# Kernel tuning notes

Hardware: AMD Instinct MI355X
Metric: run time of the kernel (lower is better)

Reference implementation:

```python
import jax, jax.numpy as jnp
import numpy as np

D_MODEL = 1024
N_HEADS = 16
HEAD = D_MODEL // N_HEADS  # 64


def setup_inputs() -> dict:
    key = jax.random.key(0)
    ks = jax.random.split(key, 9)
    s = 1.0 / np.sqrt(D_MODEL)
    x = jax.random.normal(ks[0], (2, 2048, D_MODEL), dtype=jnp.float32)
    Wq = jax.random.uniform(ks[1], (N_HEADS, D_MODEL, HEAD), jnp.float32, -s, s)
    bq = jax.random.uniform(ks[2], (N_HEADS, HEAD), jnp.float32, -s, s)
    Wk = jax.random.uniform(ks[3], (N_HEADS, D_MODEL, HEAD), jnp.float32, -s, s)
    bk = jax.random.uniform(ks[4], (N_HEADS, HEAD), jnp.float32, -s, s)
    Wv = jax.random.uniform(ks[5], (N_HEADS, D_MODEL, HEAD), jnp.float32, -s, s)
    bv = jax.random.uniform(ks[6], (N_HEADS, HEAD), jnp.float32, -s, s)
    Wo = jax.random.uniform(ks[7], (D_MODEL, D_MODEL), jnp.float32, -s, s)
    bo = jax.random.uniform(ks[8], (D_MODEL,), jnp.float32, -s, s)
    return {"x": x, "Wq": Wq, "bq": bq, "Wk": Wk, "bk": bk,
            "Wv": Wv, "bv": bv, "Wo": Wo, "bo": bo}


def reference(x, Wq, bq, Wk, bk, Wv, bv, Wo, bo):
    # Per-head projections, vectorized over heads: [B,S,D] x [H,D,h] -> [B,H,S,h]
    Q = jnp.einsum('bsd,hdk->bhsk', x, Wq) + bq[None, :, None, :]
    K = jnp.einsum('bsd,hdk->bhsk', x, Wk) + bk[None, :, None, :]
    V = jnp.einsum('bsd,hdk->bhsk', x, Wv) + bv[None, :, None, :]
    scores = jnp.einsum('bhqk,bhsk->bhqs', Q, K) / jnp.sqrt(jnp.float32(HEAD))
    attn = jax.nn.softmax(scores, axis=-1)  # dropout is identity in eval mode
    out = jnp.einsum('bhqs,bhsk->bhqk', attn, V)  # [B,H,S,h]
    B, H, S, h = out.shape
    out = out.transpose(0, 2, 1, 3).reshape(B, S, H * h)  # concat heads -> [B,S,D]
    return out @ Wo.T + bo if False else jnp.einsum('bsd,ed->bse', out, Wo.T.T) + bo
```

## Files before the change

kernel.cpp:

```cpp
#include <hip/hip_runtime.h>
#include <hip/hip_bf16.h>

typedef unsigned short u16;
typedef short short8 __attribute__((ext_vector_type(8)));
typedef float floatx4 __attribute__((ext_vector_type(4)));

#define MFMA16(a, b, c) __builtin_amdgcn_mfma_f32_16x16x32_bf16((a), (b), (c), 0, 0, 0)

union U128u { uint4 q; u16 s[8]; };

__device__ __forceinline__ u16 f2bf(float f) {
  union { float f; unsigned u; } v; v.f = f;
  unsigned r = v.u + 0x7fffu + ((v.u >> 16) & 1u);
  return (u16)(r >> 16);
}

__device__ __forceinline__ float bf2f(u16 s) {
  union { unsigned u; float f; } v; v.u = ((unsigned)s) << 16;
  return v.f;
}

__device__ __forceinline__ unsigned pk2(float hi, float lo) {
  union { float f; unsigned u; } a, b;
  a.f = hi; b.f = lo;
  return __builtin_amdgcn_perm(a.u + 0x8000u, b.u + 0x8000u, 0x07060302u);
}

__device__ __forceinline__ float fexp2(float x) {
#if __has_builtin(__builtin_amdgcn_exp2f)
  return __builtin_amdgcn_exp2f(x);
#else
  return exp2f(x);
#endif
}

__device__ __forceinline__ void async16(const u16* g, u16* l) {
  __builtin_amdgcn_global_load_lds(
      (const __attribute__((address_space(1))) unsigned int*)g,
      (__attribute__((address_space(3))) unsigned int*)l, 16, 0, 0);
}


__global__ __launch_bounds__(256) void prep_all(
    const float* __restrict__ x, const float* __restrict__ Wo,
    const float* __restrict__ Wq, const float* __restrict__ bq,
    const float* __restrict__ Wk, const float* __restrict__ bk,
    const float* __restrict__ Wv, const float* __restrict__ bv,
    u16* __restrict__ Xb, u16* __restrict__ Wob,
    u16* __restrict__ Wt, float* __restrict__ ball) {
  int bid = blockIdx.x;
  int tid = threadIdx.x;
  if (bid < 5120) {
    const float* src = bid < 4096 ? x : Wo;
    u16* dst = bid < 4096 ? Xb : Wob;
    int i = (bid < 4096 ? bid : bid - 4096) * 256 + tid;
    float4 v = ((const float4*)src)[i];
    union { unsigned long long ll; u16 s[4]; } o;
    o.s[0] = f2bf(v.x); o.s[1] = f2bf(v.y); o.s[2] = f2bf(v.z); o.s[3] = f2bf(v.w);
    ((unsigned long long*)dst)[i] = o.ll;
    return;
  }
  int id = (bid - 5120) * 256 + tid;
  int kk4 = id & 15;
  int d = (id >> 4) & 1023;
  int h = (id >> 14) & 15;
  int wsel = id >> 18;
  const float* W = wsel == 0 ? Wq : (wsel == 1 ? Wk : Wv);
  float4 v = *(const float4*)(W + ((size_t)(h * 1024 + d)) * 64 + kk4 * 4);
  int nb = wsel * 1024 + h * 64 + kk4 * 4;
  Wt[(size_t)(nb + 0) * 1024 + d] = f2bf(v.x);
  Wt[(size_t)(nb + 1) * 1024 + d] = f2bf(v.y);
  Wt[(size_t)(nb + 2) * 1024 + d] = f2bf(v.z);
  Wt[(size_t)(nb + 3) * 1024 + d] = f2bf(v.w);
  if (id < 3072) {
    int ws2 = id >> 10, hk = id & 1023;
    const float* bsrc = ws2 == 0 ? bq : (ws2 == 1 ? bk : bv);
    ball[id] = bsrc[hk];
  }
}

__global__ __launch_bounds__(256) void transpose_v(const u16* __restrict__ QKV,
                                                   u16* __restrict__ Vtc) {
  __shared__ u16 t[64][65];
  int tid = threadIdx.x;
  int bh = blockIdx.y, b = bh >> 4, h = bh & 15;
  int s0 = blockIdx.x * 64;
  int v0 = blockIdx.x * 4;
  {
    int r = tid >> 2, c0 = (tid & 3) * 16;
    const u16* src = QKV + (size_t)(b * 2048 + s0 + r) * 3072 + 2048 + h * 64 + c0;
    U128u a, c;
    a.q = *(const uint4*)src;
    c.q = *(const uint4*)(src + 8);
#pragma unroll
    for (int j = 0; j < 8; ++j) { t[r][c0 + j] = a.s[j]; t[r][c0 + 8 + j] = c.s[j]; }
  }
  __syncthreads();
  {
    int g = tid;
#pragma unroll
    for (int gg = 0; gg < 2; ++gg, g += 256) {
      int d = g & 63, o = (g >> 6) & 1, vloc = g >> 7;
      int sl = vloc * 16 + o * 8;
      U128u out;
#pragma unroll
      for (int k = 0; k < 8; ++k) out.s[k] = t[sl + k][d];
      u16* dst = Vtc + (((size_t)(bh * 128 + v0 + vloc) * 2 + o) * 64 + d) * 8;
      *(uint4*)dst = out.q;
    }
  }
}


__device__ __forceinline__ void store_out(u16* p, float v) { *p = f2bf(v); }
__device__ __forceinline__ void store_out(float* p, float v) { *p = v; }

template <int BN, typename OutT>
__global__ __launch_bounds__(256) void gemm_bt(
    const u16* __restrict__ A, const u16* __restrict__ B,
    const float* __restrict__ bias, OutT* __restrict__ C,
    int M, int N, int K, int scaleNend, float scaleVal) {
  constexpr int TN = BN / 32;
  __shared__ __attribute__((aligned(16))) u16 As[128 * 32];
  __shared__ __attribute__((aligned(16))) u16 Bs[BN * 32];
  const int tid = threadIdx.x;
  const int w = tid >> 6, lane = tid & 63;
  const int l15 = lane & 15, l4 = lane >> 4;
  const int lin = blockIdx.x;
  const int xcd = lin & 7, sblk = lin >> 3;
  const int bm = xcd * 4 + (sblk & 3);
  const int bn = sblk >> 2;
  const int wm = (w & 1) * 64, wn = (w >> 1) * (BN / 2);

  floatx4 acc[4][TN];
#pragma unroll
  for (int i = 0; i < 4; ++i)
#pragma unroll
    for (int j = 0; j < TN; ++j) acc[i][j] = (floatx4){0.f, 0.f, 0.f, 0.f};

  for (int k0 = 0; k0 < K; k0 += 32) {
    __syncthreads();
#pragma unroll
    for (int j = 0; j < 2; ++j) {
      int i = j * 256 + tid;
      int row = i >> 2, ko = (i & 3) * 8;
      async16(A + (size_t)(bm * 128 + row) * K + k0 + ko, As + (j * 256 + w * 64) * 8);
    }
#pragma unroll
    for (int j = 0; j < BN / 64; ++j) {
      int i = j * 256 + tid;
      int row = i >> 2, ko = (i & 3) * 8;
      async16(B + (size_t)(bn * BN + row) * K + k0 + ko, Bs + (j * 256 + w * 64) * 8);
    }
    __syncthreads();
    short8 af[4], bf[TN];
#pragma unroll
    for (int t = 0; t < 4; ++t)
      af[t] = *(const short8*)(As + (wm + t * 16 + l15) * 32 + l4 * 8);
#pragma unroll
    for (int t = 0; t < TN; ++t)
      bf[t] = *(const short8*)(Bs + (wn + t * 16 + l15) * 32 + l4 * 8);
#pragma unroll
    for (int tm = 0; tm < 4; ++tm)
#pragma unroll
      for (int tn = 0; tn < TN; ++tn) acc[tm][tn] = MFMA16(af[tm], bf[tn], acc[tm][tn]);
  }

#pragma unroll
  for (int tn = 0; tn < TN; ++tn) {
    int col = bn * BN + wn + tn * 16 + l15;
    float bv = bias[col];
    float sc = (col < scaleNend) ? scaleVal : 1.0f;
#pragma unroll
    for (int tm = 0; tm < 4; ++tm) {
      int row0 = bm * 128 + wm + tm * 16 + l4 * 4;
#pragma unroll
      for (int r = 0; r < 4; ++r) {
        float v = (acc[tm][tn][r] + bv) * sc;
        store_out(C + (size_t)(row0 + r) * N + col, v);
      }
    }
  }
}


__global__ __launch_bounds__(256, 3) void attn_kernel(const u16* __restrict__ QKV,
                                                      const u16* __restrict__ Vtc,
                                                      u16* __restrict__ Ob) {
  __shared__ __attribute__((aligned(16))) u16 lds[4 * 4736];
  const int tid = threadIdx.x;
  const int w = tid >> 6, lane = tid & 63;
  const int l15 = lane & 15, l4 = lane >> 4;
  const int lin = blockIdx.x;
  const int xcd = lin & 7, sblk = lin >> 3;
  const int bh = xcd * 4 + (sblk & 3);
  const int q0 = (sblk >> 2) * 64;
  const int b = bh >> 4, h = bh & 15;

  u16* const Pw = lds + w * 4736;

  short8 qf[4][2];
  {
    const u16* Qb = QKV + (size_t)(b * 2048 + q0) * 3072 + h * 64;
#pragma unroll
    for (int tq = 0; tq < 4; ++tq)
#pragma unroll
      for (int s = 0; s < 2; ++s)
        qf[tq][s] = *(const short8*)(Qb + (size_t)(tq * 16 + l15) * 3072 + s * 32 + l4 * 8);
  }

  floatx4 Oacc[4][4];
#pragma unroll
  for (int i = 0; i < 4; ++i)
#pragma unroll
    for (int j = 0; j < 4; ++j) Oacc[i][j] = (floatx4){0.f, 0.f, 0.f, 0.f};
  float lpart[4] = {0.f, 0.f, 0.f, 0.f};

  const u16* const Kb = QKV + (size_t)(b * 2048) * 3072 + 1024 + h * 64;
  const u16* const Vw = Vtc + (size_t)bh * 131072 + (size_t)w * 32768;
  const int kw0 = w * 512;

  for (int c = 0; c < 16; ++c) {
    const int key0 = kw0 + c * 32;
    short8 kf[2][2];
#pragma unroll
    for (int t = 0; t < 2; ++t)
#pragma unroll
      for (int s = 0; s < 2; ++s)
        kf[t][s] = *(const short8*)(Kb + (size_t)(key0 + t * 16 + l15) * 3072 + s * 32 + l4 * 8);
    short8 vf[4];
#pragma unroll
    for (int td = 0; td < 4; ++td)
      vf[td] = *(const short8*)(Vw + (size_t)c * 2048 + l4 * 512 + (td * 16 + l15) * 8);

#pragma unroll
    for (int t = 0; t < 2; ++t)
#pragma unroll
      for (int tq = 0; tq < 4; ++tq) {
        floatx4 s = (floatx4){0.f, 0.f, 0.f, 0.f};
        s = MFMA16(kf[t][0], qf[tq][0], s);
        s = MFMA16(kf[t][1], qf[tq][1], s);
        float p0 = fexp2(s[0]), p1 = fexp2(s[1]), p2 = fexp2(s[2]), p3 = fexp2(s[3]);
        lpart[tq] += (p0 + p1) + (p2 + p3);
        unsigned lo = pk2(p1, p0), hi = pk2(p3, p2);
        *(unsigned long long*)(Pw + (size_t)(tq * 16 + l15) * 40 + t * 16 + l4 * 4) =
            ((unsigned long long)hi << 32) | lo;
      }

    short8 pf[4];
#pragma unroll
    for (int tq = 0; tq < 4; ++tq)
      pf[tq] = *(const short8*)(Pw + (size_t)(tq * 16 + l15) * 40 + l4 * 8);
#pragma unroll
    for (int td = 0; td < 4; ++td)
#pragma unroll
      for (int tq = 0; tq < 4; ++tq) Oacc[tq][td] = MFMA16(pf[tq], vf[td], Oacc[tq][td]);
  }

  float lr[4];
#pragma unroll
  for (int tq = 0; tq < 4; ++tq) {
    float l = lpart[tq];
    l += __shfl_xor(l, 16);
    l += __shfl_xor(l, 32);
    lr[tq] = l;
  }

#pragma unroll
  for (int tq = 0; tq < 4; ++tq)
#pragma unroll
    for (int td = 0; td < 4; ++td)
#pragma unroll
      for (int r = 0; r < 4; ++r)
        Pw[(size_t)(tq * 16 + l4 * 4 + r) * 72 + td * 16 + l15] = f2bf(Oacc[tq][td][r]);
  if (l4 == 0) {
    float* Lw = (float*)(Pw + 4608);
#pragma unroll
    for (int tq = 0; tq < 4; ++tq) Lw[tq * 16 + l15] = lr[tq];
  }
  __syncthreads();

  {
    int row = tid >> 2, c0 = (tid & 3) * 16;
    float acc[16];
#pragma unroll
    for (int j = 0; j < 16; ++j) acc[j] = 0.f;
    float lsum = 0.f;
#pragma unroll
    for (int wv = 0; wv < 4; ++wv) {
      const u16* R = lds + wv * 4736;
      lsum += ((const float*)(R + 4608))[row];
      U128u x1, x2;
      x1.q = *(const uint4*)(R + (size_t)row * 72 + c0);
      x2.q = *(const uint4*)(R + (size_t)row * 72 + c0 + 8);
#pragma unroll
      for (int j = 0; j < 8; ++j) { acc[j] += bf2f(x1.s[j]); acc[8 + j] += bf2f(x2.s[j]); }
    }
    float inv = 1.0f / lsum;
    U128u o1, o2;
#pragma unroll
    for (int j = 0; j < 8; ++j) { o1.s[j] = f2bf(acc[j] * inv); o2.s[j] = f2bf(acc[8 + j] * inv); }
    u16* Op = Ob + (size_t)(b * 2048 + q0 + row) * 1024 + h * 64 + c0;
    *(uint4*)Op = o1.q;
    *(uint4*)(Op + 8) = o2.q;
  }
}


extern "C" void kernel_launch(void* const* d_in, const int* in_sizes, int n_in,
                              void* d_out, int out_size, void* d_ws, size_t ws_size,
                              hipStream_t stream) {
  const float* x  = (const float*)d_in[0];
  const float* Wq = (const float*)d_in[1];
  const float* bq = (const float*)d_in[2];
  const float* Wk = (const float*)d_in[3];
  const float* bk = (const float*)d_in[4];
  const float* Wv = (const float*)d_in[5];
  const float* bv = (const float*)d_in[6];
  const float* Wo = (const float*)d_in[7];
  const float* bo = (const float*)d_in[8];

  char* p = (char*)d_ws;
  u16* Xb   = (u16*)p; p += (size_t)4096 * 1024 * 2;
  u16* Wt   = (u16*)p; p += (size_t)3072 * 1024 * 2;
  u16* QKV  = (u16*)p; p += (size_t)4096 * 3072 * 2;
  u16* Vtc  = (u16*)p; p += (size_t)32 * 128 * 2 * 64 * 8 * 2;
  u16* Ob   = (u16*)p; p += (size_t)4096 * 1024 * 2;
  u16* Wob  = (u16*)p; p += (size_t)1024 * 1024 * 2;
  float* ball = (float*)p; p += 3072 * sizeof(float);

  const float qscale = 0.125f * 1.4426950408889634f;

  prep_all<<<8192, 256, 0, stream>>>(x, Wo, Wq, bq, Wk, bk, Wv, bv, Xb, Wob, Wt, ball);
  gemm_bt<128, u16><<<768, 256, 0, stream>>>(Xb, Wt, ball, QKV,
                                             4096, 3072, 1024, 1024, qscale);
  transpose_v<<<dim3(32, 32), 256, 0, stream>>>(QKV, Vtc);
  attn_kernel<<<1024, 256, 0, stream>>>(QKV, Vtc, Ob);
  gemm_bt<64, float><<<512, 256, 0, stream>>>(Ob, Wob, bo, (float*)d_out,
                                              4096, 1024, 1024, 0, 1.0f);
}
```

Before: 215.4 us.

## Feed softmax P directly into fp16 PV MFMA, removing LDS round-trip

```diff
diff --git a/kernel.cpp b/kernel.cpp
--- a/kernel.cpp
+++ b/kernel.cpp
@@ -4,10 +4,14 @@
 typedef unsigned short u16;
 typedef short short8 __attribute__((ext_vector_type(8)));
 typedef float floatx4 __attribute__((ext_vector_type(4)));
+typedef __fp16 half2v __attribute__((ext_vector_type(2)));
+typedef __fp16 half4v __attribute__((ext_vector_type(4)));
 
 #define MFMA16(a, b, c) __builtin_amdgcn_mfma_f32_16x16x32_bf16((a), (b), (c), 0, 0, 0)
+#define MFMA_PV(a, b, c) __builtin_amdgcn_mfma_f32_16x16x16f16((a), (b), (c), 0, 0, 0)
 
 union U128u { uint4 q; u16 s[8]; };
+union H4u { half4v h4; half2v h2[2]; unsigned u[2]; };
 
 __device__ __forceinline__ u16 f2bf(float f) {
   union { float f; unsigned u; } v; v.f = f;
@@ -18,12 +22,6 @@
 __device__ __forceinline__ float bf2f(u16 s) {
   union { unsigned u; float f; } v; v.u = ((unsigned)s) << 16;
   return v.f;
-}
-
-__device__ __forceinline__ unsigned pk2(float hi, float lo) {
-  union { float f; unsigned u; } a, b;
-  a.f = hi; b.f = lo;
-  return __builtin_amdgcn_perm(a.u + 0x8000u, b.u + 0x8000u, 0x07060302u);
 }
 
 __device__ __forceinline__ float fexp2(float x) {
@@ -80,7 +78,7 @@
 }
 
 __global__ __launch_bounds__(256) void transpose_v(const u16* __restrict__ QKV,
-                                                   u16* __restrict__ Vtc) {
+                                                   u16* __restrict__ VtF) {
   __shared__ u16 t[64][65];
   int tid = threadIdx.x;
   int bh = blockIdx.y, b = bh >> 4, h = bh & 15;
@@ -97,16 +95,19 @@
   }
   __syncthreads();
   {
-    int g = tid;
-#pragma unroll
-    for (int gg = 0; gg < 2; ++gg, g += 256) {
-      int d = g & 63, o = (g >> 6) & 1, vloc = g >> 7;
-      int sl = vloc * 16 + o * 8;
-      U128u out;
-#pragma unroll
-      for (int k = 0; k < 8; ++k) out.s[k] = t[sl + k][d];
-      u16* dst = Vtc + (((size_t)(bh * 128 + v0 + vloc) * 2 + o) * 64 + d) * 8;
-      *(uint4*)dst = out.q;
+    int d = tid & 63, vloc = tid >> 6;
+    int sl = vloc * 16;
+    u16* dst = VtF + ((size_t)(bh * 128 + v0 + vloc)) * 1024 + d * 4;
+#pragma unroll
+    for (int kq = 0; kq < 4; ++kq) {
+      float f0 = bf2f(t[sl + kq * 4 + 0][d]);
+      float f1 = bf2f(t[sl + kq * 4 + 1][d]);
+      float f2 = bf2f(t[sl + kq * 4 + 2][d]);
+      float f3 = bf2f(t[sl + kq * 4 + 3][d]);
+      union { half2v h2[2]; uint2 u2; } o;
+      o.h2[0] = __builtin_amdgcn_cvt_pkrtz(f0, f1);
+      o.h2[1] = __builtin_amdgcn_cvt_pkrtz(f2, f3);
+      *(uint2*)(dst + kq * 256) = o.u2;
     }
   }
 }
@@ -184,10 +185,10 @@
 }
 
 
-__global__ __launch_bounds__(256, 3) void attn_kernel(const u16* __restrict__ QKV,
-                                                      const u16* __restrict__ Vtc,
+__global__ __launch_bounds__(256, 4) void attn_kernel(const u16* __restrict__ QKV,
+                                                      const u16* __restrict__ VtF,
                                                       u16* __restrict__ Ob) {
-  __shared__ __attribute__((aligned(16))) u16 lds[4 * 4736];
+  __shared__ __attribute__((aligned(16))) u16 lds[4 * 2368];
   const int tid = threadIdx.x;
   const int w = tid >> 6, lane = tid & 63;
   const int l15 = lane & 15, l4 = lane >> 4;
@@ -196,103 +197,101 @@
   const int bh = xcd * 4 + (sblk & 3);
   const int q0 = (sblk >> 2) * 64;
   const int b = bh >> 4, h = bh & 15;
-
-  u16* const Pw = lds + w * 4736;
-
-  short8 qf[4][2];
+  const int qh = w >> 1, kh = w & 1;
+
+  short8 qf[2][2];
   {
-    const u16* Qb = QKV + (size_t)(b * 2048 + q0) * 3072 + h * 64;
-#pragma unroll
-    for (int tq = 0; tq < 4; ++tq)
+    const u16* Qb = QKV + (size_t)(b * 2048 + q0 + qh * 32) * 3072 + h * 64;
+#pragma unroll
+    for (int tq = 0; tq < 2; ++tq)
 #pragma unroll
       for (int s = 0; s < 2; ++s)
         qf[tq][s] = *(const short8*)(Qb + (size_t)(tq * 16 + l15) * 3072 + s * 32 + l4 * 8);
   }
 
-  floatx4 Oacc[4][4];
-#pragma unroll
-  for (int i = 0; i < 4; ++i)
+  floatx4 Oacc[2][4];
+#pragma unroll
+  for (int i = 0; i < 2; ++i)
 #pragma unroll
     for (int j = 0; j < 4; ++j) Oacc[i][j] = (floatx4){0.f, 0.f, 0.f, 0.f};
-  float lpart[4] = {0.f, 0.f, 0.f, 0.f};
-
-  const u16* const Kb = QKV + (size_t)(b * 2048) * 3072 + 1024 + h * 64;
-  const u16* const Vw = Vtc + (size_t)bh * 131072 + (size_t)w * 32768;
-  const int kw0 = w * 512;
-
-  for (int c = 0; c < 16; ++c) {
-    const int key0 = kw0 + c * 32;
+  float lpart[2] = {0.f, 0.f};
+
+  const u16* const Kb = QKV + (size_t)(b * 2048 + kh * 1024) * 3072 + 1024 + h * 64;
+  const __fp16* const Vw =
+      (const __fp16*)VtF + ((size_t)(bh * 128 + kh * 64)) * 1024;
+
+  for (int c = 0; c < 32; ++c) {
+    const int kb0 = c * 32;
     short8 kf[2][2];
 #pragma unroll
     for (int t = 0; t < 2; ++t)
 #pragma unroll
       for (int s = 0; s < 2; ++s)
-        kf[t][s] = *(const short8*)(Kb + (size_t)(key0 + t * 16 + l15) * 3072 + s * 32 + l4 * 8);
-    short8 vf[4];
-#pragma unroll
-    for (int td = 0; td < 4; ++td)
-      vf[td] = *(const short8*)(Vw + (size_t)c * 2048 + l4 * 512 + (td * 16 + l15) * 8);
-
+        kf[t][s] = *(const short8*)(Kb + (size_t)(kb0 + t * 16 + l15) * 3072 + s * 32 + l4 * 8);
+    half4v vf[2][4];
 #pragma unroll
     for (int t = 0; t < 2; ++t)
 #pragma unroll
-      for (int tq = 0; tq < 4; ++tq) {
+      for (int td = 0; td < 4; ++td)
+        vf[t][td] = *(const half4v*)(Vw + ((size_t)(c * 2 + t) * 4 + l4) * 256 +
+                                     (td * 16 + l15) * 4);
+
+#pragma unroll
+    for (int t = 0; t < 2; ++t)
+#pragma unroll
+      for (int tq = 0; tq < 2; ++tq) {
         floatx4 s = (floatx4){0.f, 0.f, 0.f, 0.f};
         s = MFMA16(kf[t][0], qf[tq][0], s);
         s = MFMA16(kf[t][1], qf[tq][1], s);
         float p0 = fexp2(s[0]), p1 = fexp2(s[1]), p2 = fexp2(s[2]), p3 = fexp2(s[3]);
         lpart[tq] += (p0 + p1) + (p2 + p3);
-        unsigned lo = pk2(p1, p0), hi = pk2(p3, p2);
-        *(unsigned long long*)(Pw + (size_t)(tq * 16 + l15) * 40 + t * 16 + l4 * 4) =
-            ((unsigned long long)hi << 32) | lo;
+        H4u pa;
+        pa.h2[0] = __builtin_amdgcn_cvt_pkrtz(p0, p1);
+        pa.h2[1] = __builtin_amdgcn_cvt_pkrtz(p2, p3);
+#pragma unroll
+        for (int td = 0; td < 4; ++td)
+          Oacc[tq][td] = MFMA_PV(pa.h4, vf[t][td], Oacc[tq][td]);
       }
-
-    short8 pf[4];
-#pragma unroll
-    for (int tq = 0; tq < 4; ++tq)
-      pf[tq] = *(const short8*)(Pw + (size_t)(tq * 16 + l15) * 40 + l4 * 8);
-#pragma unroll
-    for (int td = 0; td < 4; ++td)
-#pragma unroll
-      for (int tq = 0; tq < 4; ++tq) Oacc[tq][td] = MFMA16(pf[tq], vf[td], Oacc[tq][td]);
-  }
-
-  float lr[4];
-#pragma unroll
-  for (int tq = 0; tq < 4; ++tq) {
+  }
+
+  float lr[2];
+#pragma unroll
+  for (int tq = 0; tq < 2; ++tq) {
     float l = lpart[tq];
     l += __shfl_xor(l, 16);
     l += __shfl_xor(l, 32);
     lr[tq] = l;
   }
 
-#pragma unroll
-  for (int tq = 0; tq < 4; ++tq)
+  u16* const Pw = lds + w * 2368;
+#pragma unroll
+  for (int tq = 0; tq < 2; ++tq)
 #pragma unroll
     for (int td = 0; td < 4; ++td)
 #pragma unroll
       for (int r = 0; r < 4; ++r)
         Pw[(size_t)(tq * 16 + l4 * 4 + r) * 72 + td * 16 + l15] = f2bf(Oacc[tq][td][r]);
   if (l4 == 0) {
-    float* Lw = (float*)(Pw + 4608);
-#pragma unroll
-    for (int tq = 0; tq < 4; ++tq) Lw[tq * 16 + l15] = lr[tq];
+    float* Lw = (float*)(Pw + 2304);
+#pragma unroll
+    for (int tq = 0; tq < 2; ++tq) Lw[tq * 16 + l15] = lr[tq];
   }
   __syncthreads();
 
   {
     int row = tid >> 2, c0 = (tid & 3) * 16;
+    int qh2 = row >> 5, r32 = row & 31;
     float acc[16];
 #pragma unroll
     for (int j = 0; j < 16; ++j) acc[j] = 0.f;
     float lsum = 0.f;
 #pragma unroll
-    for (int wv = 0; wv < 4; ++wv) {
-      const u16* R = lds + wv * 4736;
-      lsum += ((const float*)(R + 4608))[row];
+    for (int kv = 0; kv < 2; ++kv) {
+      const u16* R = lds + (qh2 * 2 + kv) * 2368;
+      lsum += ((const float*)(R + 2304))[r32];
       U128u x1, x2;
-      x1.q = *(const uint4*)(R + (size_t)row * 72 + c0);
-      x2.q = *(const uint4*)(R + (size_t)row * 72 + c0 + 8);
+      x1.q = *(const uint4*)(R + (size_t)r32 * 72 + c0);
+      x2.q = *(const uint4*)(R + (size_t)r32 * 72 + c0 + 8);
 #pragma unroll
       for (int j = 0; j < 8; ++j) { acc[j] += bf2f(x1.s[j]); acc[8 + j] += bf2f(x2.s[j]); }
     }
@@ -324,7 +323,7 @@
   u16* Xb   = (u16*)p; p += (size_t)4096 * 1024 * 2;
   u16* Wt   = (u16*)p; p += (size_t)3072 * 1024 * 2;
   u16* QKV  = (u16*)p; p += (size_t)4096 * 3072 * 2;
-  u16* Vtc  = (u16*)p; p += (size_t)32 * 128 * 2 * 64 * 8 * 2;
+  u16* VtF  = (u16*)p; p += (size_t)32 * 128 * 1024 * 2;
   u16* Ob   = (u16*)p; p += (size_t)4096 * 1024 * 2;
   u16* Wob  = (u16*)p; p += (size_t)1024 * 1024 * 2;
   float* ball = (float*)p; p += 3072 * sizeof(float);
@@ -334,8 +333,8 @@
   prep_all<<<8192, 256, 0, stream>>>(x, Wo, Wq, bq, Wk, bk, Wv, bv, Xb, Wob, Wt, ball);
   gemm_bt<128, u16><<<768, 256, 0, stream>>>(Xb, Wt, ball, QKV,
                                              4096, 3072, 1024, 1024, qscale);
-  transpose_v<<<dim3(32, 32), 256, 0, stream>>>(QKV, Vtc);
-  attn_kernel<<<1024, 256, 0, stream>>>(QKV, Vtc, Ob);
+  transpose_v<<<dim3(32, 32), 256, 0, stream>>>(QKV, VtF);
+  attn_kernel<<<1024, 256, 0, stream>>>(QKV, VtF, Ob);
   gemm_bt<64, float><<<512, 256, 0, stream>>>(Ob, Wob, bo, (float*)d_out,
                                               4096, 1024, 1024, 0, 1.0f);
 }
```

After: 245.1 us. +13.8%, slower.
